# Kernel tuning notes

Measured on AMD Instinct MI355X. Metric: run time of the kernel, lower is better.

Reference implementation:

```python
import jax, jax.numpy as jnp
import numpy as np

NEG_SLOPE = 0.2


def gat_layer(x, src, dst, W, a_src, a_dst, b, concat):
    # x: [N, F_in], W: [F_in, H*C], a_src/a_dst: [H, C], b: [H*C] or [C]
    N = x.shape[0]
    H, C = a_src.shape
    h = (x @ W).reshape(N, H, C)                       # per-head projections
    al_s = jnp.einsum('nhc,hc->nh', h, a_src)          # [N, H]
    al_d = jnp.einsum('nhc,hc->nh', h, a_dst)          # [N, H]
    e = jax.nn.leaky_relu(al_s[src] + al_d[dst], NEG_SLOPE)  # [E, H]
    # softmax over incoming edges of each destination node
    m = jax.ops.segment_max(e, dst, num_segments=N)    # [N, H]
    ex = jnp.exp(e - m[dst])
    s = jax.ops.segment_sum(ex, dst, num_segments=N)   # [N, H]
    alpha = ex / (s[dst] + 1e-16)                      # [E, H]
    msg = h[src] * alpha[:, :, None]                   # [E, H, C]
    out = jax.ops.segment_sum(msg, dst, num_segments=N)  # [N, H, C]
    out = out.reshape(N, H * C) if concat else out.mean(axis=1)
    return out + b


def setup_inputs() -> dict:
    key = jax.random.key(0)
    ks = jax.random.split(key, 12)
    N, E, F_in, HID, H, NCLS = 100000, 1600000, 128, 32, 4, 40
    x = jax.random.normal(ks[0], (N, F_in), dtype=jnp.float32)
    edge_index = jax.random.randint(ks[1], (2, E), 0, N, dtype=jnp.int32)
    W1 = jax.random.normal(ks[2], (F_in, H * HID), dtype=jnp.float32) * 0.1
    as1 = jax.random.normal(ks[3], (H, HID), dtype=jnp.float32) * 0.1
    ad1 = jax.random.normal(ks[4], (H, HID), dtype=jnp.float32) * 0.1
    b1 = jnp.zeros((H * HID,), dtype=jnp.float32)
    W2 = jax.random.normal(ks[5], (H * HID, H * NCLS), dtype=jnp.float32) * 0.1
    as2 = jax.random.normal(ks[6], (H, NCLS), dtype=jnp.float32) * 0.1
    ad2 = jax.random.normal(ks[7], (H, NCLS), dtype=jnp.float32) * 0.1
    b2 = jnp.zeros((NCLS,), dtype=jnp.float32)
    return {"x": x, "edge_index": edge_index, "W1": W1, "as1": as1,
            "ad1": ad1, "b1": b1, "W2": W2, "as2": as2, "ad2": ad2, "b2": b2}


def reference(x, edge_index, W1, as1, ad1, b1, W2, as2, ad2, b2):
    src, dst = edge_index[0], edge_index[1]
    h = gat_layer(x, src, dst, W1, as1, ad1, b1, concat=True)
    h = jax.nn.relu(h)  # dropout=0.0 -> identity
    out = gat_layer(h, src, dst, W2, as2, ad2, b2, concat=False)
    return jax.nn.log_softmax(out, axis=-1)
```

## Files before the change

### kernel.cpp

```cpp
#include <hip/hip_runtime.h>

typedef short short8 __attribute__((ext_vector_type(8)));
typedef float f32x4 __attribute__((ext_vector_type(4)));
typedef int   i32x4 __attribute__((ext_vector_type(4)));
typedef unsigned short u16;
typedef unsigned int u32;

__device__ __forceinline__ float b2f(u16 u){ union{u32 i; float f;} v; v.i=((u32)u)<<16; return v.f; }
__device__ __forceinline__ u16 f2b(float f){ union{float f; u32 i;} v; v.f=f; return (u16)((v.i + 0x7fffu + ((v.i>>16)&1u))>>16); }
__device__ __forceinline__ float loadv(const void* p, long i, bool isbf){
  return isbf ? b2f(((const u16*)p)[i]) : ((const float*)p)[i];
}

__global__ void detect_bf16(const void* x, int n, int* flag){
  __shared__ int cnt;
  if (threadIdx.x==0) cnt = 0;
  __syncthreads();
  int m = n < 4096 ? n : 4096;
  int good = 0;
  for (int i = threadIdx.x; i < m; i += 256){
    u16 u = ((const u16*)x)[i];
    int e = (u >> 7) & 0xff;
    if (u == 0 || (e >= 100 && e <= 140)) good++;
  }
  atomicAdd(&cnt, good);
  __syncthreads();
  if (threadIdx.x==0){
    flag[0] = (cnt >= (m*3)/4) ? 1 : 0;
    flag[1] = 1;
  }
}

__global__ __launch_bounds__(256) void init_k(const void* __restrict__ W1, const void* __restrict__ W2,
                                              u16* __restrict__ WT1, u16* __restrict__ WT2,
                                              int* __restrict__ counts, int N, const int* __restrict__ flag){
  const bool wbf = *flag != 0;
  int gid = blockIdx.x*256 + threadIdx.x;
  if (gid < 128*128){
    int i = gid, k = i >> 7, c = i & 127;
    WT1[c*128 + k] = wbf ? ((const u16*)W1)[i] : f2b(((const float*)W1)[i]);
  } else if (gid < 128*128 + 128*160){
    int i = gid - 128*128, k = i / 160, c = i - k*160;
    WT2[c*128 + k] = wbf ? ((const u16*)W2)[i] : f2b(((const float*)W2)[i]);
  } else {
    int i = gid - (128*128 + 128*160);
    if (i < N) counts[i] = 0;
  }
}

__global__ __launch_bounds__(256) void count_x(const int* __restrict__ dst,
    int* __restrict__ counts, int E, int N, int nchunk){
  int r = blockIdx.x & 7;
  int chunk = blockIdx.x >> 3;
  int lo = (int)(((long)N * r) >> 3);
  int hi = (int)(((long)N * (r+1)) >> 3);
  int per = (E + nchunk - 1) / nchunk;
  int s = chunk * per, t = min(E, s + per);
  for (int e = s + threadIdx.x; e < t; e += 256){
    int d = dst[e];
    if (d >= lo && d < hi) atomicAdd(&counts[d], 1);
  }
}

__global__ __launch_bounds__(256) void scatter_x(const int* __restrict__ src, const int* __restrict__ dst,
    const int* __restrict__ rp, int* __restrict__ cur,
    int* __restrict__ psrc, int E, int N, int nchunk){
  int r = blockIdx.x & 7;
  int chunk = blockIdx.x >> 3;
  int lo = (int)(((long)N * r) >> 3);
  int hi = (int)(((long)N * (r+1)) >> 3);
  int per = (E + nchunk - 1) / nchunk;
  int s = chunk * per, t = min(E, s + per);
  for (int e = s + threadIdx.x; e < t; e += 256){
    int d = dst[e];
    if (d >= lo && d < hi){
      int pos = rp[d] + atomicAdd(&cur[d], 1);
      psrc[pos] = src[e];
    }
  }
}

__global__ __launch_bounds__(256) void scan_bsum(const int* __restrict__ counts, int* __restrict__ bsum, int N){
  __shared__ int sm[256];
  int t = threadIdx.x, i = blockIdx.x*256 + t;
  sm[t] = (i < N) ? counts[i] : 0;
  __syncthreads();
  for (int off = 128; off; off >>= 1){
    if (t < off) sm[t] += sm[t+off];
    __syncthreads();
  }
  if (t == 0) bsum[blockIdx.x] = sm[0];
}

__global__ __launch_bounds__(1024) void scan_top(const int* __restrict__ bsum, int* __restrict__ bscan, int B){
  __shared__ int sm[1024];
  int t = threadIdx.x;
  int v = (t < B) ? bsum[t] : 0;
  sm[t] = v;
  __syncthreads();
  for (int off = 1; off < 1024; off <<= 1){
    int x = (t >= off) ? sm[t-off] : 0;
    __syncthreads();
    sm[t] += x;
    __syncthreads();
  }
  if (t < B) bscan[t] = sm[t] - v;
}

__global__ __launch_bounds__(256) void scan_final(const int* __restrict__ counts_in, int* __restrict__ counts_clr,
                                                  const int* __restrict__ bscan,
                                                  int* __restrict__ rp, int N, int E){
  __shared__ int sm[256];
  int t = threadIdx.x, i = blockIdx.x*256 + t;
  int v = (i < N) ? counts_in[i] : 0;
  sm[t] = v;
  __syncthreads();
  for (int off = 1; off < 256; off <<= 1){
    int x = (t >= off) ? sm[t-off] : 0;
    __syncthreads();
    sm[t] += x;
    __syncthreads();
  }
  if (i < N){ rp[i] = bscan[blockIdx.x] + sm[t] - v; counts_clr[i] = 0; }
  if (i == 0) rp[N] = E;
}

template<int M, int C>
__global__ __launch_bounds__(256) void gemm_al(const void* __restrict__ X, const u16* __restrict__ WT,
                                               const void* __restrict__ as_, const void* __restrict__ ad_,
                                               u16* __restrict__ OUT, u16* __restrict__ OUT2,
                                               float* __restrict__ als, float* __restrict__ ald,
                                               int N, const int* __restrict__ flagX, const int* __restrict__ flagW){
  __shared__ u16 wt[M][136];
  __shared__ float s_as[4*C], s_ad[4*C];
  const bool xbf = *flagX != 0;
  const bool abf = *flagW != 0;
  int tid = threadIdx.x;
  for (int i = tid; i < M*16; i += 256){
    int c = i >> 4, k8 = (i & 15) << 3;
    *(short8*)&wt[c][k8] = *(const short8*)&WT[c*128 + k8];
  }
  for (int i = tid; i < 4*C; i += 256){
    s_as[i] = loadv(as_, i, abf);
    s_ad[i] = loadv(ad_, i, abf);
  }
  __syncthreads();
  int wave = tid >> 6, lane = tid & 63;
  int quad = lane >> 4, l16 = lane & 15;
  int rowbase = blockIdx.x*64 + wave*16;
  int rr = rowbase + l16; if (rr >= N) rr = N-1;
  const int NT = M/16;
  f32x4 acc[NT];
  #pragma unroll
  for (int t=0;t<NT;t++) acc[t] = (f32x4){0.f,0.f,0.f,0.f};
  #pragma unroll
  for (int kt = 0; kt < 4; kt++){
    int kb = kt*32 + quad*8;
    short8 a;
    if (xbf){
      a = *(const short8*)((const u16*)X + (size_t)rr*128 + kb);
    } else {
      const float* xf = (const float*)X + (size_t)rr*128 + kb;
      #pragma unroll
      for (int j=0;j<8;j++) a[j] = (short)f2b(xf[j]);
    }
    #pragma unroll
    for (int t=0;t<NT;t++){
      short8 b = *(const short8*)&wt[t*16 + l16][kb];
      acc[t] = __builtin_amdgcn_mfma_f32_16x16x32_bf16(a, b, acc[t], 0, 0, 0);
    }
  }
  #pragma unroll
  for (int t=0;t<NT;t++){
    #pragma unroll
    for (int r=0;r<4;r++){
      int row = rowbase + quad*4 + r;
      if (row < N){
        u16 val = f2b(acc[t][r]);
        if (M > 128 && t*16 >= 128) OUT2[(size_t)row*32 + (t*16 - 128) + l16] = val;
        else                        OUT [(size_t)row*128 + t*16 + l16]        = val;
      }
    }
  }
  float ps[4][4], pd[4][4];
  #pragma unroll
  for (int r=0;r<4;r++)
    #pragma unroll
    for (int h=0;h<4;h++){ ps[r][h]=0.f; pd[r][h]=0.f; }
  #pragma unroll
  for (int t=0;t<NT;t++){
    const int hlo = (t*16)/C;
    const int hhi = (t*16+15)/C;
    int col = t*16 + l16;
    float avs = s_as[col], avd = s_ad[col];
    if (hlo == hhi){
      #pragma unroll
      for (int r=0;r<4;r++){ ps[r][hlo] += acc[t][r]*avs; pd[r][hlo] += acc[t][r]*avd; }
    } else {
      if (l16 < hhi*C - t*16){
        #pragma unroll
        for (int r=0;r<4;r++){ ps[r][hlo] += acc[t][r]*avs; pd[r][hlo] += acc[t][r]*avd; }
      } else {
        #pragma unroll
        for (int r=0;r<4;r++){ ps[r][hhi] += acc[t][r]*avs; pd[r][hhi] += acc[t][r]*avd; }
      }
    }
  }
  #pragma unroll
  for (int off=1; off<16; off<<=1){
    #pragma unroll
    for (int r=0;r<4;r++)
      #pragma unroll
      for (int h=0;h<4;h++){
        ps[r][h] += __shfl_xor(ps[r][h], off);
        pd[r][h] += __shfl_xor(pd[r][h], off);
      }
  }
  float vs = 0.f, vd = 0.f;
  #pragma unroll
  for (int r=0;r<4;r++)
    #pragma unroll
    for (int h=0;h<4;h++)
      if (l16 == r*4 + h){ vs = ps[r][h]; vd = pd[r][h]; }
  int wrow = rowbase + quad*4 + (l16 >> 2);
  if (wrow < N){
    als[wrow*4 + (l16 & 3)] = vs;
    ald[wrow*4 + (l16 & 3)] = vd;
  }
}

__global__ __launch_bounds__(256) void agg1(const u16* __restrict__ h1,
    const float* __restrict__ als, const float* __restrict__ ald, const void* __restrict__ b1,
    const int* __restrict__ rp, const int* __restrict__ psrc,
    u16* __restrict__ hrelu, int N, const int* __restrict__ flag){
  __shared__ __align__(16) int   sbuf[4][16];
  __shared__ __align__(16) float ebT[4][4*20];
  const bool isbf = *flag != 0;
  int wave = threadIdx.x >> 6, lane = threadIdx.x & 63;
  int node = blockIdx.x*4 + wave;
  bool live = node < N;
  int nd = live ? node : 0;
  int hd = lane >> 4;
  int eidx = lane >> 2, hA = lane & 3;
  int beg = __builtin_amdgcn_readfirstlane(rp[nd]);
  int end = __builtin_amdgcn_readfirstlane(rp[nd+1]);
  if (!live){ beg = 0; end = 0; }
  float advA = ald[nd*4 + hA];
  const char* hb = (const char*)h1;
  int lane4 = lane << 2;
  int* sb = sbuf[wave];
  float* eb = ebT[wave];
  float a0 = 0.f, a1 = 0.f;
  float sp = 0.f;
  for (int cbeg = beg; cbeg < end; cbeg += 16){
    int cnt = min(16, end - cbeg);
    int e = cbeg + eidx;
    bool vv = e < end;
    int ec = vv ? e : beg;
    int s = psrc[ec];
    float lv = als[s*4 + hA] + advA;
    lv = fmaxf(lv, 0.2f*lv);
    float ex = vv ? __expf(lv) : 0.f;
    sp += ex;
    eb[hA*20 + eidx] = ex;
    if (hA == 0) sb[eidx] = vv ? (s << 8) : 0;
    for (int j0 = 0; j0 < cnt; j0 += 4){
      i32x4 off4 = *(const i32x4*)&sb[j0];
      f32x4 ex4  = *(const f32x4*)&eb[hd*20 + j0];
      u32 p[4];
      #pragma unroll
      for (int i=0;i<4;i++) p[i] = *(const u32*)(hb + (u32)(off4[i] + lane4));
      #pragma unroll
      for (int i=0;i<4;i++){
        union{u32 u; float f;} w;
        w.u = p[i] << 16;         a0 += ex4[i]*w.f;
        w.u = p[i] & 0xffff0000u; a1 += ex4[i]*w.f;
      }
    }
  }
  sp += __shfl_xor(sp, 4);  sp += __shfl_xor(sp, 8);
  sp += __shfl_xor(sp, 16); sp += __shfl_xor(sp, 32);
  float sum = __shfl(sp, hd);
  if (live){
    float inv = 1.f/(sum + 1e-16f);
    float v0 = a0*inv + loadv(b1, 2*lane,     isbf);
    float v1 = a1*inv + loadv(b1, 2*lane + 1, isbf);
    v0 = v0 > 0.f ? v0 : 0.f;
    v1 = v1 > 0.f ? v1 : 0.f;
    u32 packed = (u32)f2b(v0) | ((u32)f2b(v1) << 16);
    *(u32*)(hrelu + (size_t)node*128 + 2*lane) = packed;
  }
}

__global__ __launch_bounds__(256) void agg2(const u16* __restrict__ h2m, const u16* __restrict__ h2t,
    const float* __restrict__ als, const float* __restrict__ ald, const void* __restrict__ b2,
    const int* __restrict__ rp, const int* __restrict__ psrc,
    void* __restrict__ out, int N, const int* __restrict__ flag){
  __shared__ __align__(16) int   sbuf[4][16];
  __shared__ __align__(16) float ebT[4][4*20];
  __shared__ __align__(16) float sm[4][160];
  const bool isbf = *flag != 0;
  int wave = threadIdx.x >> 6, lane = threadIdx.x & 63;
  int node = blockIdx.x*4 + wave;
  bool live = node < N;
  int nd = live ? node : 0;
  int g = lane >> 4, s = lane & 15;
  int hm = s / 5;
  int moff = s << 4;
  int tof  = s << 2;
  int eidx = lane >> 2, hA = lane & 3;
  int beg = __builtin_amdgcn_readfirstlane(rp[nd]);
  int end = __builtin_amdgcn_readfirstlane(rp[nd+1]);
  if (!live){ beg = 0; end = 0; }
  float advA = ald[nd*4 + hA];
  const char* hbm = (const char*)h2m;
  const char* hbt = (const char*)h2t;
  int* sb = sbuf[wave];
  float* eb = ebT[wave];
  float am[8] = {0.f,0.f,0.f,0.f,0.f,0.f,0.f,0.f};
  float at0 = 0.f, at1 = 0.f;
  float sp = 0.f;
  for (int cbeg = beg; cbeg < end; cbeg += 16){
    int cnt = min(16, end - cbeg);
    int e = cbeg + eidx;
    bool vv = e < end;
    int ec = vv ? e : beg;
    int src = psrc[ec];
    float lv = als[src*4 + hA] + advA;
    lv = fmaxf(lv, 0.2f*lv);
    float ex = vv ? __expf(lv) : 0.f;
    sp += ex;
    eb[hA*20 + eidx] = ex;
    if (hA == 0) sb[eidx] = vv ? src : 0;
    for (int j0 = 0; j0 < cnt; j0 += 4){
      int sv    = sb[j0 + g];
      float exm = eb[hm*20 + j0 + g];
      float ext = eb[3*20  + j0 + g];
      i32x4 P = *(const i32x4*)(hbm + ((((u32)sv) << 8) + moff));
      u32   q = *(const u32*) (hbt + ((((u32)sv) << 6) + tof));
      union{u32 u; float f;} w;
      #pragma unroll
      for (int i=0;i<4;i++){
        u32 pv = (u32)P[i];
        w.u = pv << 16;         am[2*i]   += exm*w.f;
        w.u = pv & 0xffff0000u; am[2*i+1] += exm*w.f;
      }
      w.u = q << 16;         at0 += ext*w.f;
      w.u = q & 0xffff0000u; at1 += ext*w.f;
    }
  }
  sp += __shfl_xor(sp, 4);  sp += __shfl_xor(sp, 8);
  sp += __shfl_xor(sp, 16); sp += __shfl_xor(sp, 32);
  float Sm = __shfl(sp, hm);
  float S3 = __shfl(sp, 3);
  #pragma unroll
  for (int k=0;k<8;k++){ am[k] += __shfl_xor(am[k],16); am[k] += __shfl_xor(am[k],32); }
  at0 += __shfl_xor(at0,16); at0 += __shfl_xor(at0,32);
  at1 += __shfl_xor(at1,16); at1 += __shfl_xor(at1,32);
  if (lane < 16){
    float invm = 1.f/(Sm + 1e-16f);
    float invt = 1.f/(S3 + 1e-16f);
    f32x4 v0 = {am[0]*invm, am[1]*invm, am[2]*invm, am[3]*invm};
    f32x4 v1 = {am[4]*invm, am[5]*invm, am[6]*invm, am[7]*invm};
    *(f32x4*)&sm[wave][8*s]     = v0;
    *(f32x4*)&sm[wave][8*s + 4] = v1;
    sm[wave][128 + 2*s] = at0*invt;
    sm[wave][129 + 2*s] = at1*invt;
  }
  __syncthreads();
  float v = -__builtin_inff();
  if (lane < 40)
    v = (sm[wave][lane] + sm[wave][40+lane] + sm[wave][80+lane] + sm[wave][120+lane]) * 0.25f
        + loadv(b2, lane, isbf);
  float mxo = v;
  for (int o = 32; o; o >>= 1) mxo = fmaxf(mxo, __shfl_xor(mxo, o));
  float exl = (lane < 40) ? __expf(v - mxo) : 0.f;
  float S = exl;
  for (int o = 32; o; o >>= 1) S += __shfl_xor(S, o);
  if (live && lane < 40){
    float r = v - mxo - __logf(S);
    if (isbf) ((u16*)out)[(size_t)node*40 + lane] = f2b(r);
    else      ((float*)out)[(size_t)node*40 + lane] = r;
  }
}

extern "C" void kernel_launch(void* const* d_in, const int* in_sizes, int n_in,
                              void* d_out, int out_size, void* d_ws, size_t ws_size,
                              hipStream_t stream){
  const void* x   = d_in[0];
  const int*  ei  = (const int*)d_in[1];
  const void* W1  = d_in[2];
  const void* as1 = d_in[3];
  const void* ad1 = d_in[4];
  const void* b1  = d_in[5];
  const void* W2  = d_in[6];
  const void* as2 = d_in[7];
  const void* ad2 = d_in[8];
  const void* b2  = d_in[9];

  const int N = in_sizes[0] / 128;
  const int E = in_sizes[1] / 2;
  const int* esrc = ei;
  const int* edst = ei + E;

  char* w = (char*)d_ws;
  size_t off = 0;
  auto take = [&](size_t bytes)->void*{
    void* p = w + off;
    off = (off + bytes + 255) & ~(size_t)255;
    return p;
  };
  u16*   h12    = (u16*)take((size_t)N*128*2);
  u16*   h2t    = (u16*)take((size_t)N*32*2);
  u16*   hrelu  = (u16*)take((size_t)N*128*2);
  float* als1   = (float*)take((size_t)N*4*4);
  float* ald1   = (float*)take((size_t)N*4*4);
  float* als2   = (float*)take((size_t)N*4*4);
  float* ald2   = (float*)take((size_t)N*4*4);
  int*   rowptr = (int*)take((size_t)(N+1)*4);
  int*   counts = (int*)take((size_t)N*4);
  int*   bsum   = (int*)take(1024*4);
  int*   bscan  = (int*)take(1024*4);
  int*   psrc   = (int*)take((size_t)E*4);
  int*   flag   = (int*)take(64);
  u16*   wt1    = (u16*)take(128*128*2);
  u16*   wt2    = (u16*)take(160*128*2);

  const int B = (N + 255) / 256;
  const int NCHUNK = 128;
  const int INIT_W = 128*128 + 128*160;

  detect_bf16<<<1, 256, 0, stream>>>(x, N*128, flag);
  init_k<<<(INIT_W + N + 255)/256, 256, 0, stream>>>(W1, W2, wt1, wt2, counts, N, flag);

  count_x<<<8*NCHUNK, 256, 0, stream>>>(edst, counts, E, N, NCHUNK);
  scan_bsum<<<B, 256, 0, stream>>>(counts, bsum, N);
  scan_top<<<1, 1024, 0, stream>>>(bsum, bscan, B);
  scan_final<<<B, 256, 0, stream>>>(counts, counts, bscan, rowptr, N, E);
  scatter_x<<<8*NCHUNK, 256, 0, stream>>>(esrc, edst, rowptr, counts, psrc, E, N, NCHUNK);

  gemm_al<128,32><<<(N+63)/64, 256, 0, stream>>>(x, wt1, as1, ad1, h12, h2t ,
                                                 als1, ald1, N, flag, flag);
  agg1<<<(N+3)/4, 256, 0, stream>>>(h12, als1, ald1, b1, rowptr, psrc, hrelu, N, flag);

  gemm_al<160,40><<<(N+63)/64, 256, 0, stream>>>(hrelu, wt2, as2, ad2, h12, h2t,
                                                 als2, ald2, N, flag+1, flag);
  agg2<<<(N+3)/4, 256, 0, stream>>>(h12, h2t, als2, ald2, b2, rowptr, psrc, d_out, N, flag);
}
```

Baseline: 480.4 us.

## Fuse edge scatter and first-layer GEMM into one interleaved kernel launch

```diff
diff --git a/kernel.cpp b/kernel.cpp
--- a/kernel.cpp
+++ b/kernel.cpp
@@ -62,24 +62,6 @@
   }
 }
 
-__global__ __launch_bounds__(256) void scatter_x(const int* __restrict__ src, const int* __restrict__ dst,
-    const int* __restrict__ rp, int* __restrict__ cur,
-    int* __restrict__ psrc, int E, int N, int nchunk){
-  int r = blockIdx.x & 7;
-  int chunk = blockIdx.x >> 3;
-  int lo = (int)(((long)N * r) >> 3);
-  int hi = (int)(((long)N * (r+1)) >> 3);
-  int per = (E + nchunk - 1) / nchunk;
-  int s = chunk * per, t = min(E, s + per);
-  for (int e = s + threadIdx.x; e < t; e += 256){
-    int d = dst[e];
-    if (d >= lo && d < hi){
-      int pos = rp[d] + atomicAdd(&cur[d], 1);
-      psrc[pos] = src[e];
-    }
-  }
-}
-
 __global__ __launch_bounds__(256) void scan_bsum(const int* __restrict__ counts, int* __restrict__ bsum, int N){
   __shared__ int sm[256];
   int t = threadIdx.x, i = blockIdx.x*256 + t;
@@ -123,6 +105,117 @@
   }
   if (i < N){ rp[i] = bscan[blockIdx.x] + sm[t] - v; counts_clr[i] = 0; }
   if (i == 0) rp[N] = E;
+}
+
+__global__ __launch_bounds__(256) void scat_gemm1(
+    const int* __restrict__ esrc, const int* __restrict__ edst,
+    const int* __restrict__ rp, int* __restrict__ cur, int* __restrict__ psrc,
+    int E, int nchunk,
+    const void* __restrict__ X, const u16* __restrict__ WT,
+    const void* __restrict__ as_, const void* __restrict__ ad_,
+    u16* __restrict__ OUT, float* __restrict__ als, float* __restrict__ ald,
+    int N, const int* __restrict__ flagX, const int* __restrict__ flagW){
+  __shared__ u16 wt[128][136];
+  __shared__ float s_as[128], s_ad[128];
+  int b = blockIdx.x;
+  int two = 2*8*nchunk;
+  if (b < two && (((b >> 3) & 1) == 0)){
+    int r = b & 7;
+    int chunk = b >> 4;
+    int lo = (int)(((long)N * r) >> 3);
+    int hi = (int)(((long)N * (r+1)) >> 3);
+    int per = (E + nchunk - 1) / nchunk;
+    int s = chunk * per, t = min(E, s + per);
+    for (int e = s + threadIdx.x; e < t; e += 256){
+      int d = edst[e];
+      if (d >= lo && d < hi){
+        int pos = rp[d] + atomicAdd(&cur[d], 1);
+        psrc[pos] = esrc[e];
+      }
+    }
+    return;
+  }
+  int bid = (b < two) ? ((b >> 4)*8 + (b & 7)) : (8*nchunk + (b - two));
+  int NT1 = (N + 63) >> 6;
+  if (bid >= NT1) return;
+  const bool xbf = *flagX != 0;
+  const bool abf = *flagW != 0;
+  int tid = threadIdx.x;
+  for (int i = tid; i < 128*16; i += 256){
+    int c = i >> 4, k8 = (i & 15) << 3;
+    *(short8*)&wt[c][k8] = *(const short8*)&WT[c*128 + k8];
+  }
+  for (int i = tid; i < 128; i += 256){
+    s_as[i] = loadv(as_, i, abf);
+    s_ad[i] = loadv(ad_, i, abf);
+  }
+  __syncthreads();
+  int wave = tid >> 6, lane = tid & 63;
+  int quad = lane >> 4, l16 = lane & 15;
+  int rowbase = bid*64 + wave*16;
+  int rr = rowbase + l16; if (rr >= N) rr = N-1;
+  f32x4 acc[8];
+  #pragma unroll
+  for (int t=0;t<8;t++) acc[t] = (f32x4){0.f,0.f,0.f,0.f};
+  #pragma unroll
+  for (int kt = 0; kt < 4; kt++){
+    int kb = kt*32 + quad*8;
+    short8 a;
+    if (xbf){
+      a = *(const short8*)((const u16*)X + (size_t)rr*128 + kb);
+    } else {
+      const float* xf = (const float*)X + (size_t)rr*128 + kb;
+      #pragma unroll
+      for (int j=0;j<8;j++) a[j] = (short)f2b(xf[j]);
+    }
+    #pragma unroll
+    for (int t=0;t<8;t++){
+      short8 bb = *(const short8*)&wt[t*16 + l16][kb];
+      acc[t] = __builtin_amdgcn_mfma_f32_16x16x32_bf16(a, bb, acc[t], 0, 0, 0);
+    }
+  }
+  #pragma unroll
+  for (int t=0;t<8;t++){
+    #pragma unroll
+    for (int r=0;r<4;r++){
+      int row = rowbase + quad*4 + r;
+      if (row < N) OUT[(size_t)row*128 + t*16 + l16] = f2b(acc[t][r]);
+    }
+  }
+  float ps[4][4], pd[4][4];
+  #pragma unroll
+  for (int r=0;r<4;r++)
+    #pragma unroll
+    for (int h=0;h<4;h++){ ps[r][h]=0.f; pd[r][h]=0.f; }
+  #pragma unroll
+  for (int t=0;t<8;t++){
+    const int hh = t >> 1;
+    int col = t*16 + l16;
+    float avs = s_as[col], avd = s_ad[col];
+    #pragma unroll
+    for (int r=0;r<4;r++){ ps[r][hh] += acc[t][r]*avs; pd[r][hh] += acc[t][r]*avd; }
+  }
+  #pragma unroll
+  for (int off=1; off<16; off<<=1){
+    #pragma unroll
+    for (int r=0;r<4;r++)
+      #pragma unroll
+      for (int h=0;h<4;h++){
+        ps[r][h] += __shfl_xor(ps[r][h], off);
+        pd[r][h] += __shfl_xor(pd[r][h], off);
+      }
+  }
+  float vs = 0.f, vd = 0.f;
+  #pragma unroll
+  for (int r=0;r<4;r++)
+    #pragma unroll
+    for (int h=0;h<4;h++)
+      if (l16 == r*4 + h){ vs = ps[r][h]; vd = pd[r][h]; }
+  int wrow = rowbase + quad*4 + (l16 >> 2);
+  if (wrow < N){
+    als[wrow*4 + (l16 & 3)] = vs;
+    ald[wrow*4 + (l16 & 3)] = vd;
+  }
 }
 
 template<int M, int C>
@@ -437,10 +530,12 @@
   scan_bsum<<<B, 256, 0, stream>>>(counts, bsum, N);
   scan_top<<<1, 1024, 0, stream>>>(bsum, bscan, B);
   scan_final<<<B, 256, 0, stream>>>(counts, counts, bscan, rowptr, N, E);
-  scatter_x<<<8*NCHUNK, 256, 0, stream>>>(esrc, edst, rowptr, counts, psrc, E, N, NCHUNK);
-
-  gemm_al<128,32><<<(N+63)/64, 256, 0, stream>>>(x, wt1, as1, ad1, h12, h2t ,
-                                                 als1, ald1, N, flag, flag);
+
+  const int NT1 = (N + 63) / 64;
+  const int SGGRID = 2*8*NCHUNK + (NT1 > 8*NCHUNK ? NT1 - 8*NCHUNK : 0);
+  scat_gemm1<<<SGGRID, 256, 0, stream>>>(esrc, edst, rowptr, counts, psrc, E, NCHUNK,
+                                         x, wt1, as1, ad1, h12, als1, ald1, N, flag, flag);
+
   agg1<<<(N+3)/4, 256, 0, stream>>>(h12, als1, ald1, b1, rowptr, psrc, hrelu, N, flag);
 
   gemm_al<160,40><<<(N+63)/64, 256, 0, stream>>>(hrelu, wt2, as2, ad2, h12, h2t,
```

New measurement: 509.9 us. +6.1%, slower.
